# Performance work log

Hardware: AMD Instinct MI355X
Metric: run time of the kernel (lower is better)

## Reference

```python
import jax, jax.numpy as jnp
import numpy as np

B = 8            # graphs per batch (batch_size)
NPG = 4096       # nodes per graph
EPG = 65536      # edges per graph (avg degree 16)
IN = 384
K1, K2, K3 = 2458, 1475, 738   # ceil(.6*4096), ceil(.6*2458), ceil(.5*1475)
EPS = 1e-5


def setup_inputs() -> dict:
    key = jax.random.key(0)
    ks = jax.random.split(key, 16)
    x = jax.random.normal(ks[0], (B * NPG, IN), jnp.float32)
    off = (jnp.arange(B, dtype=jnp.int32) * NPG)[:, None]
    src = jax.random.randint(ks[1], (B, EPG), 0, NPG, dtype=jnp.int32) + off
    dst = jax.random.randint(ks[2], (B, EPG), 0, NPG, dtype=jnp.int32) + off
    edge_index = jnp.stack([src.reshape(-1), dst.reshape(-1)])

    def lin(k, i, o):
        return jax.random.normal(k, (i, o), jnp.float32) / np.sqrt(i)

    return dict(
        x=x, edge_index=edge_index,
        W1=lin(ks[3], IN, 512), b1=jnp.zeros(512, jnp.float32),
        W2=lin(ks[4], 512, 512), b2=jnp.zeros(512, jnp.float32),
        W3=lin(ks[5], 512, 256), b3=jnp.zeros(256, jnp.float32),
        W4=lin(ks[6], 256, 192), b4=jnp.zeros(192, jnp.float32),
        g1=jnp.ones(512, jnp.float32), be1=jnp.zeros(512, jnp.float32),
        g2=jnp.ones(512, jnp.float32), be2=jnp.zeros(512, jnp.float32),
        g3=jnp.ones(256, jnp.float32), be3=jnp.zeros(256, jnp.float32),
        p1_wrel=lin(ks[7], 512, 1), p1_brel=jnp.zeros(1, jnp.float32), p1_wroot=lin(ks[8], 512, 1),
        p2_wrel=lin(ks[9], 512, 1), p2_brel=jnp.zeros(1, jnp.float32), p2_wroot=lin(ks[10], 512, 1),
        p3_wrel=lin(ks[11], 256, 1), p3_brel=jnp.zeros(1, jnp.float32), p3_wroot=lin(ks[12], 256, 1),
    )


def _gcn_conv(x, W, b, src, dst, em, n):
    # PyG GCNConv(add_self_loops=False): h = D^-1/2 A D^-1/2 (x W) + b
    h = x @ W
    deg = jax.ops.segment_sum(em, dst, num_segments=n)           # in-degree of valid edges
    dis = jnp.where(deg > 0, jax.lax.rsqrt(jnp.maximum(deg, 1e-12)), 0.0)
    norm = (dis[src] * dis[dst] * em)[:, None]
    return jax.ops.segment_sum(h[src] * norm, dst, num_segments=n) + b


def _bn(x, g, b):
    # BatchNorm(track_running_stats=False): always batch stats, biased var
    mu = jnp.mean(x, axis=0)
    var = jnp.mean(jnp.square(x - mu), axis=0)
    return (x - mu) * jax.lax.rsqrt(var + EPS) * g + b


def _sag_score(x, wrel, brel, wroot, src, dst, em, n):
    # SAGPooling's GNN = GraphConv: lin_rel(sum_j x_j) + lin_root(x)
    agg = jax.ops.segment_sum(x[src] * em[:, None], dst, num_segments=n)
    return (agg @ wrel + brel + x @ wroot)[:, 0]


def _sag_pool(x, score, src, dst, em, npg, k):
    # per-graph top-k on raw scores; kept features scaled by tanh(score)
    topv, topi = jax.lax.top_k(score.reshape(B, npg), k)
    perm = (topi + (jnp.arange(B, dtype=jnp.int32) * npg)[:, None]).reshape(-1)
    xn = x[perm] * jnp.tanh(topv.reshape(-1))[:, None]
    inv = jnp.full(B * npg, -1, jnp.int32).at[perm].set(
        jnp.arange(B * k, dtype=jnp.int32))
    ns, nd = inv[src], inv[dst]
    keep = (ns >= 0) & (nd >= 0)
    em = em * keep.astype(x.dtype)
    return xn, jnp.where(keep, ns, 0), jnp.where(keep, nd, 0), em


def reference(x, edge_index,
              W1, b1, W2, b2, W3, b3, W4, b4,
              g1, be1, g2, be2, g3, be3,
              p1_wrel, p1_brel, p1_wroot,
              p2_wrel, p2_brel, p2_wroot,
              p3_wrel, p3_brel, p3_wroot,
              batch_size=8):
    src, dst = edge_index[0], edge_index[1]
    em = jnp.ones(src.shape[0], x.dtype)

    h = jax.nn.relu(_bn(_gcn_conv(x, W1, b1, src, dst, em, B * NPG), g1, be1))
    s = _sag_score(h, p1_wrel, p1_brel, p1_wroot, src, dst, em, B * NPG)
    h, src, dst, em = _sag_pool(h, s, src, dst, em, NPG, K1)

    h = jax.nn.relu(_bn(_gcn_conv(h, W2, b2, src, dst, em, B * K1), g2, be2))
    s = _sag_score(h, p2_wrel, p2_brel, p2_wroot, src, dst, em, B * K1)
    h, src, dst, em = _sag_pool(h, s, src, dst, em, K1, K2)

    h = jax.nn.relu(_bn(_gcn_conv(h, W3, b3, src, dst, em, B * K2), g3, be3))
    s = _sag_score(h, p3_wrel, p3_brel, p3_wroot, src, dst, em, B * K2)
    h, src, dst, em = _sag_pool(h, s, src, dst, em, K2, K3)

    h = _gcn_conv(h, W4, b4, src, dst, em, B * K3)      # [B*K3, 192]
    hg = h.reshape(B, K3, 192)
    return jnp.mean(hg, axis=1) + jnp.max(hg, axis=1)   # global mean + max pool
```

## Files before the change

kernel.cpp:

```cpp
#include <hip/hip_runtime.h>
#include <cmath>

#define E_TOTAL 524288
#define NB 8

using f32x4 = __attribute__((ext_vector_type(4))) float;
using s16x8 = __attribute__((ext_vector_type(8))) short;
using s16x4 = __attribute__((ext_vector_type(4))) short;

static inline int cdiv(int a, int b) { return (a + b - 1) / b; }

__device__ inline unsigned short bf16_rn(float x) {
  unsigned u = __float_as_uint(x);
  return (unsigned short)((u + 0x7FFFu + ((u >> 16) & 1u)) >> 16);
}
__device__ inline void split3(float x, short& h, short& m, short& l) {
  unsigned short hb = bf16_rn(x);
  h = (short)hb;
  float hf = __uint_as_float(((unsigned)hb) << 16);
  float r1 = x - hf;
  unsigned short mb = bf16_rn(r1);
  m = (short)mb;
  float mf = __uint_as_float(((unsigned)mb) << 16);
  l = (short)bf16_rn(r1 - mf);
}

__device__ inline void async_copy16(const short* g, short* l) {
  __builtin_amdgcn_global_load_lds(
      (const __attribute__((address_space(1))) void*)(unsigned long long)(g),
      (__attribute__((address_space(3))) void*)(unsigned)(unsigned long long)(l),
      16, 0, 0);
}

__global__ void fill_i32(int* p, int v, int n) {
  int i = blockIdx.x * 256 + threadIdx.x;
  if (i < n) p[i] = v;
}

__global__ void split_w_t(const float* __restrict__ W, short* __restrict__ TH,
                          short* __restrict__ TM, short* __restrict__ TL, int K, int N) {
  int i = blockIdx.x * 256 + threadIdx.x;
  if (i >= K * N) return;
  int k = i / N, n = i % N;
  short h, m, l;
  split3(W[i], h, m, l);
  TH[(size_t)n * K + k] = h;
  TM[(size_t)n * K + k] = m;
  TL[(size_t)n * K + k] = l;
}

#define GBM 128
#define GBN 256
#define GBK 32
#define BUFS 36864
#define BOFF 12288

__global__ __launch_bounds__(512) void gemm_mfma(
    const short* __restrict__ AH, const short* __restrict__ AM, const short* __restrict__ AL,
    const short* __restrict__ BH, const short* __restrict__ BM, const short* __restrict__ BL,
    const float* __restrict__ bias, float* __restrict__ C,
    int M, int K, int N, int nblocks) {
  __shared__ __align__(16) short lds[2][BUFS];
  int nwg = gridDim.x;
  int orig = blockIdx.x;
  int q = nwg >> 3, r = nwg & 7;
  int xc = orig & 7, j8 = orig >> 3;
  int wg = (xc < r ? xc * (q + 1) : r * (q + 1) + (xc - r) * q) + j8;
  int bm = (wg / nblocks) * GBM;
  int bn = (wg % nblocks) * GBN;
  int tid = threadIdx.x;
  int wave = tid >> 6, lane = tid & 63;
  int wr = wave >> 2, wc = wave & 3;
  int l15 = lane & 15, l4 = lane >> 4;
  int pa = wave * 64 + lane;
  int ra = pa >> 2, ca = (pa & 3) ^ ((ra >> 1) & 3);
  int gar = bm + ra; gar = gar < M ? gar : 0;
  size_t gaoff = (size_t)gar * K + ca * 8;
  int adest = wave * 512;
  int pb0 = wave * 128 + lane, pb1 = pb0 + 64;
  int rb0 = pb0 >> 2, cb0 = (pb0 & 3) ^ ((rb0 >> 1) & 3);
  int rb1 = pb1 >> 2, cb1 = (pb1 & 3) ^ ((rb1 >> 1) & 3);
  int gbr0 = bn + rb0; gbr0 = gbr0 < N ? gbr0 : 0;
  int gbr1 = bn + rb1; gbr1 = gbr1 < N ? gbr1 : 0;
  size_t gboff0 = (size_t)gbr0 * K + cb0 * 8;
  size_t gboff1 = (size_t)gbr1 * K + cb1 * 8;
  int bdest = BOFF + wave * 1024;

  auto stage = [&](int b, int k0) {
    short* base = lds[b];
    async_copy16(AH + gaoff + k0, base + adest);
    async_copy16(AM + gaoff + k0, base + 4096 + adest);
    async_copy16(AL + gaoff + k0, base + 8192 + adest);
    async_copy16(BH + gboff0 + k0, base + bdest);
    async_copy16(BH + gboff1 + k0, base + bdest + 512);
    async_copy16(BM + gboff0 + k0, base + 8192 + bdest);
    async_copy16(BM + gboff1 + k0, base + 8192 + bdest + 512);
    async_copy16(BL + gboff0 + k0, base + 16384 + bdest);
    async_copy16(BL + gboff1 + k0, base + 16384 + bdest + 512);
  };

  f32x4 acc[4][4] = {};
  int cur = 0;
  stage(0, 0);
  __syncthreads();
  for (int k0 = 0; k0 < K; k0 += GBK) {
    if (k0 + GBK < K) stage(cur ^ 1, k0 + GBK);
    const short* base = lds[cur];
    s16x8 fah[4], fam[4], fal[4], fbh[4], fbm[4], fbl[4];
#pragma unroll
    for (int mi = 0; mi < 4; ++mi) {
      int row = wr * 64 + mi * 16 + l15;
      int ad = row * 32 + ((l4 ^ ((row >> 1) & 3)) << 3);
      fah[mi] = *(const s16x8*)(base + ad);
      fam[mi] = *(const s16x8*)(base + 4096 + ad);
      fal[mi] = *(const s16x8*)(base + 8192 + ad);
    }
#pragma unroll
    for (int ni = 0; ni < 4; ++ni) {
      int row = wc * 64 + ni * 16 + l15;
      int bd = BOFF + row * 32 + ((l4 ^ ((row >> 1) & 3)) << 3);
      fbh[ni] = *(const s16x8*)(base + bd);
      fbm[ni] = *(const s16x8*)(base + 8192 + bd);
      fbl[ni] = *(const s16x8*)(base + 16384 + bd);
    }
#pragma unroll
    for (int mi = 0; mi < 4; ++mi)
#pragma unroll
      for (int ni = 0; ni < 4; ++ni) {
        acc[mi][ni] = __builtin_amdgcn_mfma_f32_16x16x32_bf16(fah[mi], fbh[ni], acc[mi][ni], 0, 0, 0);
        acc[mi][ni] = __builtin_amdgcn_mfma_f32_16x16x32_bf16(fah[mi], fbm[ni], acc[mi][ni], 0, 0, 0);
        acc[mi][ni] = __builtin_amdgcn_mfma_f32_16x16x32_bf16(fam[mi], fbh[ni], acc[mi][ni], 0, 0, 0);
        acc[mi][ni] = __builtin_amdgcn_mfma_f32_16x16x32_bf16(fah[mi], fbl[ni], acc[mi][ni], 0, 0, 0);
        acc[mi][ni] = __builtin_amdgcn_mfma_f32_16x16x32_bf16(fal[mi], fbh[ni], acc[mi][ni], 0, 0, 0);
        acc[mi][ni] = __builtin_amdgcn_mfma_f32_16x16x32_bf16(fam[mi], fbm[ni], acc[mi][ni], 0, 0, 0);
      }
    __syncthreads();
    cur ^= 1;
  }
#pragma unroll
  for (int ni = 0; ni < 4; ++ni) {
    int col = bn + wc * 64 + ni * 16 + l15;
    if (col >= N) continue;
    float bv = bias ? bias[col] : 0.f;
#pragma unroll
    for (int mi = 0; mi < 4; ++mi) {
      int row0 = bm + wr * 64 + mi * 16 + l4 * 4;
#pragma unroll
      for (int rr = 0; rr < 4; ++rr) {
        int row = row0 + rr;
        if (row < M) C[(size_t)row * N + col] = acc[mi][ni][rr] + bv;
      }
    }
  }
}

__global__ void count_kernel(const int* __restrict__ dst, int* __restrict__ cnt, int E) {
  int e = blockIdx.x * 256 + threadIdx.x;
  if (e >= E) return;
  atomicAdd(&cnt[dst[e]], 1);
}

__global__ __launch_bounds__(1024) void scan_kernel(const int* __restrict__ cnt,
                                                    int* __restrict__ offs,
                                                    float* __restrict__ dis, int n) {
  __shared__ int tsum[1024];
  int tid = threadIdx.x;
  int chunk = (n + 1023) / 1024;
  int base = tid * chunk;
  int lsum = 0;
  for (int i = 0; i < chunk; ++i) {
    int idx = base + i;
    if (idx < n) lsum += cnt[idx];
  }
  tsum[tid] = lsum;
  __syncthreads();
  for (int off = 1; off < 1024; off <<= 1) {
    int add = (tid >= off) ? tsum[tid - off] : 0;
    __syncthreads();
    tsum[tid] += add;
    __syncthreads();
  }
  int run = (tid == 0) ? 0 : tsum[tid - 1];
  for (int i = 0; i < chunk; ++i) {
    int idx = base + i;
    if (idx < n) {
      offs[idx] = run;
      int c = cnt[idx];
      run += c;
      dis[idx] = (c > 0) ? (float)(1.0 / sqrt((double)c)) : 0.f;
    }
  }
  if (tid == 1023) offs[n] = run;
}

__global__ void scatter_kernel(const int* __restrict__ src, const int* __restrict__ dst,
                               const int* __restrict__ offs, int* __restrict__ tmpc,
                               int* __restrict__ esrc, int E) {
  int e = blockIdx.x * 256 + threadIdx.x;
  if (e >= E) return;
  int d = dst[e];
  if (d < 0) return;
  int pos = offs[d] + atomicAdd(&tmpc[d], 1);
  esrc[pos] = src[e];
}

__global__ void sort_buckets(const int* __restrict__ offs, int* __restrict__ esrc, int n) {
  int node = blockIdx.x * 256 + threadIdx.x;
  if (node >= n) return;
  int s0 = offs[node], s1 = offs[node + 1];
  for (int i = s0 + 1; i < s1; ++i) {
    int v = esrc[i];
    int j = i - 1;
    while (j >= s0 && esrc[j] > v) { esrc[j + 1] = esrc[j]; --j; }
    esrc[j + 1] = v;
  }
}

__global__ __launch_bounds__(256) void agg_kernel(
    const float* __restrict__ h, const int* __restrict__ offs,
    const int* __restrict__ esrc, const float* __restrict__ dis,
    const float* __restrict__ bias, float* __restrict__ outf,
    short* __restrict__ outh, short* __restrict__ outm, short* __restrict__ outl,
    int F, int n) {
  int node = blockIdx.x * 4 + (threadIdx.x >> 6);
  if (node >= n) return;
  int lane = threadIdx.x & 63;
  int nf4 = F >> 2;
  int i0 = lane, i1 = lane + 64;
  bool a0 = i0 < nf4, a1 = i1 < nf4;
  f32x4 acc0 = {}, acc1 = {};
  int e0 = offs[node], e1 = offs[node + 1];
  int e = e0;
  for (; e + 4 <= e1; e += 4) {
    int s0 = esrc[e], s1 = esrc[e + 1], s2 = esrc[e + 2], s3 = esrc[e + 3];
    float w0 = dis[s0], w1 = dis[s1], w2 = dis[s2], w3 = dis[s3];
    const f32x4* p0 = (const f32x4*)(h + (size_t)s0 * F);
    const f32x4* p1 = (const f32x4*)(h + (size_t)s1 * F);
    const f32x4* p2 = (const f32x4*)(h + (size_t)s2 * F);
    const f32x4* p3 = (const f32x4*)(h + (size_t)s3 * F);
    if (a0) {
      f32x4 v0 = p0[i0], v1 = p1[i0], v2 = p2[i0], v3 = p3[i0];
      acc0 += v0 * w0;
      acc0 += v1 * w1;
      acc0 += v2 * w2;
      acc0 += v3 * w3;
    }
    if (a1) {
      f32x4 v0 = p0[i1], v1 = p1[i1], v2 = p2[i1], v3 = p3[i1];
      acc1 += v0 * w0;
      acc1 += v1 * w1;
      acc1 += v2 * w2;
      acc1 += v3 * w3;
    }
  }
  for (; e < e1; ++e) {
    int s = esrc[e];
    float w = dis[s];
    const f32x4* hp = (const f32x4*)(h + (size_t)s * F);
    if (a0) acc0 += hp[i0] * w;
    if (a1) acc1 += hp[i1] * w;
  }
  float wd = dis[node];
  acc0 *= wd;
  acc1 *= wd;
  if (outf) {
    const f32x4* b4 = (const f32x4*)bias;
    f32x4* op = (f32x4*)(outf + (size_t)node * F);
    if (a0) op[i0] = acc0 + b4[i0];
    if (a1) op[i1] = acc1 + b4[i1];
  } else {
    short hh[4], mm[4], ll[4];
    if (a0) {
#pragma unroll
      for (int c = 0; c < 4; ++c) split3(acc0[c], hh[c], mm[c], ll[c]);
      *(s16x4*)&outh[(size_t)node * F + i0 * 4] = *(s16x4*)hh;
      *(s16x4*)&outm[(size_t)node * F + i0 * 4] = *(s16x4*)mm;
      *(s16x4*)&outl[(size_t)node * F + i0 * 4] = *(s16x4*)ll;
    }
    if (a1) {
#pragma unroll
      for (int c = 0; c < 4; ++c) split3(acc1[c], hh[c], mm[c], ll[c]);
      *(s16x4*)&outh[(size_t)node * F + i1 * 4] = *(s16x4*)hh;
      *(s16x4*)&outm[(size_t)node * F + i1 * 4] = *(s16x4*)mm;
      *(s16x4*)&outl[(size_t)node * F + i1 * 4] = *(s16x4*)ll;
    }
  }
}

#define BNY 512
__global__ void bn_stats_part(const float* __restrict__ x, double* __restrict__ psum,
                              double* __restrict__ psq, int n, int F) {
  int col = blockIdx.x * 256 + threadIdx.x;
  if (col >= F) return;
  double s = 0., q = 0.;
  for (int r = blockIdx.y; r < n; r += gridDim.y) {
    double v = (double)x[(size_t)r * F + col];
    s += v;
    q += v * v;
  }
  psum[blockIdx.y * F + col] = s;
  psq[blockIdx.y * F + col] = q;
}

__global__ __launch_bounds__(64) void bn_reduce(
    const double* __restrict__ psum, const double* __restrict__ psq,
    const float* __restrict__ g, const float* __restrict__ be,
    float* __restrict__ scf, float* __restrict__ shf,
    double* __restrict__ scd, double* __restrict__ shd, int n, int F) {
  int c = blockIdx.x;
  int lane = threadIdx.x;
  double s = 0., q = 0.;
  for (int p = lane; p < BNY; p += 64) {
    s += psum[p * F + c];
    q += psq[p * F + c];
  }
#pragma unroll
  for (int o = 1; o < 64; o <<= 1) {
    s += __shfl_xor(s, o, 64);
    q += __shfl_xor(q, o, 64);
  }
  if (lane == 0) {
    double inv_n = 1.0 / (double)n;
    double mu = s * inv_n;
    double var = q * inv_n - mu * mu;
    if (var < 0.) var = 0.;
    double istd = 1.0 / sqrt(var + 1e-5);
    double sc = istd * (double)g[c];
    double sh = (double)be[c] - mu * sc;
    scd[c] = sc;
    shd[c] = sh;
    scf[c] = (float)sc;
    shf[c] = (float)sh;
  }
}

__global__ __launch_bounds__(256) void bn_apply_score(
    float* __restrict__ hx, const float* __restrict__ scf, const float* __restrict__ shf,
    const double* __restrict__ scd, const double* __restrict__ shd,
    const float* __restrict__ wrel, const float* __restrict__ wroot,
    double* __restrict__ t, double* __restrict__ r, int F, int n) {
  int row = blockIdx.x * 4 + (threadIdx.x >> 6);
  if (row >= n) return;
  int lane = threadIdx.x & 63;
  int nf4 = F >> 2;
  f32x4* hp = (f32x4*)(hx + (size_t)row * F);
  const f32x4* sc = (const f32x4*)scf;
  const f32x4* sh = (const f32x4*)shf;
  double dr = 0., dq = 0.;
  for (int j = lane; j < nf4; j += 64) {
    f32x4 hv = hp[j];
    f32x4 v = hv * sc[j] + sh[j];
#pragma unroll
    for (int c = 0; c < 4; ++c) v[c] = fmaxf(v[c], 0.f);
    hp[j] = v;
#pragma unroll
    for (int c = 0; c < 4; ++c) {
      double vd = (double)hv[c] * scd[j * 4 + c] + shd[j * 4 + c];
      vd = vd > 0. ? vd : 0.;
      dr += vd * (double)wrel[j * 4 + c];
      dq += vd * (double)wroot[j * 4 + c];
    }
  }
#pragma unroll
  for (int o = 1; o < 64; o <<= 1) {
    dr += __shfl_xor(dr, o, 64);
    dq += __shfl_xor(dq, o, 64);
  }
  if (lane == 0) { t[row] = dr; r[row] = dq; }
}

__global__ void score_kernel(const int* __restrict__ offs, const int* __restrict__ esrc,
                             const double* __restrict__ t, const double* __restrict__ r,
                             const float* __restrict__ brel, double* __restrict__ s, int n) {
  int i = blockIdx.x * 256 + threadIdx.x;
  if (i >= n) return;
  double acc = 0.;
  int e0 = offs[i], e1 = offs[i + 1];
  for (int e = e0; e < e1; ++e) acc += t[esrc[e]];
  s[i] = acc + r[i] + (double)brel[0];
}

__global__ __launch_bounds__(1024) void topk_kernel(
    const double* __restrict__ s, int n_pg, int k, int npad,
    int* __restrict__ perm, float* __restrict__ tanhv, int* __restrict__ inv) {
  extern __shared__ char smem[];
  unsigned long long* sk = (unsigned long long*)smem;
  unsigned* si = (unsigned*)(smem + (size_t)npad * 8);
  int g = blockIdx.x;
  for (int i = threadIdx.x; i < n_pg; i += blockDim.x)
    inv[(size_t)g * n_pg + i] = -1;
  for (int i = threadIdx.x; i < npad; i += blockDim.x) {
    if (i < n_pg) {
      double v = s[(size_t)g * n_pg + i];
      unsigned long long u = (unsigned long long)__double_as_longlong(v);
      u = (u >> 63) ? ~u : (u | 0x8000000000000000ULL);
      sk[i] = ~u;
      si[i] = (unsigned)i;
    } else {
      sk[i] = 0xFFFFFFFFFFFFFFFFULL;
      si[i] = 0xFFFFFFFFu;
    }
  }
  __syncthreads();
  for (int size = 2; size <= npad; size <<= 1) {
    for (int stride = size >> 1; stride > 0; stride >>= 1) {
      for (int t = threadIdx.x; t < (npad >> 1); t += blockDim.x) {
        int i = ((t / stride) * stride * 2) + (t % stride);
        int j = i + stride;
        bool up = ((i & size) == 0);
        unsigned long long ka = sk[i], kb = sk[j];
        unsigned ia = si[i], ib = si[j];
        bool sw = up ? ((ka > kb) || (ka == kb && ia > ib))
                     : ((ka < kb) || (ka == kb && ia < ib));
        if (sw) { sk[i] = kb; sk[j] = ka; si[i] = ib; si[j] = ia; }
      }
      __syncthreads();
    }
  }
  for (int j = threadIdx.x; j < k; j += blockDim.x) {
    int li = (int)si[j];
    int old_g = g * n_pg + li;
    int new_g = g * k + j;
    perm[new_g] = old_g;
    tanhv[new_g] = (float)tanh(s[old_g]);
    inv[old_g] = new_g;
  }
}

__global__ __launch_bounds__(256) void gather_split(
    const float* __restrict__ h, const int* __restrict__ perm,
    const float* __restrict__ tanhv, short* __restrict__ gh, short* __restrict__ gm,
    short* __restrict__ gl, int F, int nk) {
  int i = blockIdx.x * 4 + (threadIdx.x >> 6);
  if (i >= nk) return;
  int lane = threadIdx.x & 63;
  int nf4 = F >> 2;
  int p = perm[i];
  float tv = tanhv[i];
  const f32x4* hp = (const f32x4*)(h + (size_t)p * F);
  for (int j = lane; j < nf4; j += 64) {
    f32x4 v = hp[j] * tv;
    short hh[4], mm[4], ll[4];
#pragma unroll
    for (int c = 0; c < 4; ++c) split3(v[c], hh[c], mm[c], ll[c]);
    *(s16x4*)&gh[(size_t)i * F + j * 4] = *(s16x4*)hh;
    *(s16x4*)&gm[(size_t)i * F + j * 4] = *(s16x4*)mm;
    *(s16x4*)&gl[(size_t)i * F + j * 4] = *(s16x4*)ll;
  }
}

__global__ void remap_kernel(const int* __restrict__ src_in, const int* __restrict__ dst_in,
                             const int* __restrict__ inv, int* __restrict__ src_out,
                             int* __restrict__ dst_out, int* __restrict__ cnt, int E) {
  int e = blockIdx.x * 256 + threadIdx.x;
  if (e >= E) return;
  int d = dst_in[e];
  int ns = -1, nd = -1;
  if (d >= 0) { ns = inv[src_in[e]]; nd = inv[d]; }
  if (ns >= 0 && nd >= 0) {
    src_out[e] = ns;
    dst_out[e] = nd;
    atomicAdd(&cnt[nd], 1);
  } else {
    src_out[e] = 0;
    dst_out[e] = -1;
  }
}

#define PCH 16
__global__ void pool_partial(const float* __restrict__ h, float* __restrict__ part,
                             int k3, int F) {
  int g = blockIdx.x, c = blockIdx.y;
  int tid = threadIdx.x;
  int chunk = (k3 + PCH - 1) / PCH;
  int r0 = c * chunk, r1 = min(r0 + chunk, k3);
  const float* base = h + (size_t)g * k3 * F;
  float sm = 0.f, mx = -INFINITY;
  for (int r = r0; r < r1; ++r) {
    float v = base[(size_t)r * F + tid];
    sm += v;
    mx = fmaxf(mx, v);
  }
  float* pp = part + (size_t)(g * PCH + c) * 2 * F;
  pp[tid] = sm;
  pp[F + tid] = mx;
}
__global__ void pool_final(const float* __restrict__ part, float* __restrict__ out,
                           int k3, int F) {
  int g = blockIdx.x;
  int tid = threadIdx.x;
  float sm = 0.f, mx = -INFINITY;
  for (int c = 0; c < PCH; ++c) {
    const float* pp = part + (size_t)(g * PCH + c) * 2 * F;
    sm += pp[tid];
    mx = fmaxf(mx, pp[F + tid]);
  }
  out[g * F + tid] = sm / (float)k3 + mx;
}

extern "C" void kernel_launch(void* const* d_in, const int* in_sizes, int n_in,
                              void* d_out, int out_size, void* d_ws, size_t ws_size,
                              hipStream_t stream) {
  const float* x0 = (const float*)d_in[0];
  const int* eidx = (const int*)d_in[1];
  const float* W1 = (const float*)d_in[2];  const float* b1 = (const float*)d_in[3];
  const float* W2 = (const float*)d_in[4];  const float* b2 = (const float*)d_in[5];
  const float* W3 = (const float*)d_in[6];  const float* b3 = (const float*)d_in[7];
  const float* W4 = (const float*)d_in[8];  const float* b4 = (const float*)d_in[9];
  const float* g1 = (const float*)d_in[10]; const float* be1 = (const float*)d_in[11];
  const float* g2 = (const float*)d_in[12]; const float* be2 = (const float*)d_in[13];
  const float* g3 = (const float*)d_in[14]; const float* be3 = (const float*)d_in[15];
  const float* p1r = (const float*)d_in[16]; const float* p1b = (const float*)d_in[17];
  const float* p1o = (const float*)d_in[18];
  const float* p2r = (const float*)d_in[19]; const float* p2b = (const float*)d_in[20];
  const float* p2o = (const float*)d_in[21];
  const float* p3r = (const float*)d_in[22]; const float* p3b = (const float*)d_in[23];
  const float* p3o = (const float*)d_in[24];

  char* w = (char*)d_ws;
  size_t off = 0;
  auto alloc = [&](size_t bytes) -> void* {
    void* p = w + off;
    off = (off + bytes + 255) & ~(size_t)255;
    return p;
  };
  float* BUF0 = (float*)alloc(32768ull * 512 * 4);
  float* BUF1 = (float*)alloc(19664ull * 512 * 4);
  short* XH = (short*)alloc(32768ull * 384 * 2);
  short* XM = (short*)alloc(32768ull * 384 * 2);
  short* XL = (short*)alloc(32768ull * 384 * 2);
  short* WTH = (short*)alloc(638976ull * 2);
  short* WTM = (short*)alloc(638976ull * 2);
  short* WTL = (short*)alloc(638976ull * 2);
  int* czone = (int*)alloc(65537ull * 4);
  int* cnt = czone;
  int* tmpc = czone + 32769;
  int* offs = (int*)alloc(32769 * 4);
  float* dis = (float*)alloc(32768 * 4);
  double* tvec = (double*)alloc(32768 * 8);
  double* rvec = (double*)alloc(32768 * 8);
  double* svec = (double*)alloc(32768 * 8);
  int* inv = (int*)alloc(32768 * 4);
  int* perm = (int*)alloc(32768 * 4);
  float* tanhv = (float*)alloc(32768 * 4);
  int* e0s = (int*)alloc(E_TOTAL * 4);
  int* e0d = (int*)alloc(E_TOTAL * 4);
  int* e1s = (int*)alloc(E_TOTAL * 4);
  int* e1d = (int*)alloc(E_TOTAL * 4);
  int* esrc = (int*)alloc(E_TOTAL * 4);
  double* bnsum = (double*)alloc((size_t)BNY * 512 * 8);
  double* bnsq = (double*)alloc((size_t)BNY * 512 * 8);
  float* bnscf = (float*)alloc(512 * 4);
  float* bnshf = (float*)alloc(512 * 4);
  double* bnscd = (double*)alloc(512 * 8);
  double* bnshd = (double*)alloc(512 * 8);
  float* part = (float*)alloc((size_t)NB * PCH * 2 * 192 * 4);

  const int EB = cdiv(E_TOTAL, 256);

  auto build_csr = [&](const int* src, const int* dst, int n) {
    scan_kernel<<<1, 1024, 0, stream>>>(cnt, offs, dis, n);
    scatter_kernel<<<EB, 256, 0, stream>>>(src, dst, offs, tmpc, esrc, E_TOTAL);
    sort_buckets<<<cdiv(n, 256), 256, 0, stream>>>(offs, esrc, n);
  };

  auto pool = [&](float* hbuf, int n, int n_pg, int k, int npad, int F,
                  const float* g, const float* be, const float* wr, const float* wb,
                  const float* wo, const int* src, const int* dst, int* nsrc, int* ndst) {
    bn_stats_part<<<dim3(cdiv(F, 256), BNY), 256, 0, stream>>>(hbuf, bnsum, bnsq, n, F);
    bn_reduce<<<F, 64, 0, stream>>>(bnsum, bnsq, g, be, bnscf, bnshf, bnscd, bnshd, n, F);
    bn_apply_score<<<cdiv(n, 4), 256, 0, stream>>>(hbuf, bnscf, bnshf, bnscd, bnshd, wr, wo, tvec, rvec, F, n);
    score_kernel<<<cdiv(n, 256), 256, 0, stream>>>(offs, esrc, tvec, rvec, wb, svec, n);
    topk_kernel<<<NB, 1024, (size_t)npad * 12, stream>>>(svec, n_pg, k, npad, perm, tanhv, inv);
    gather_split<<<cdiv(NB * k, 4), 256, 0, stream>>>(hbuf, perm, tanhv, XH, XM, XL, F, NB * k);
    fill_i32<<<cdiv(65537, 256), 256, 0, stream>>>(czone, 0, 65537);
    remap_kernel<<<EB, 256, 0, stream>>>(src, dst, inv, nsrc, ndst, cnt, E_TOTAL);
  };

  split_w_t<<<cdiv(384 * 512, 256), 256, 0, stream>>>(W1, WTH, WTM, WTL, 384, 512);
  split_w_t<<<cdiv(512 * 512, 256), 256, 0, stream>>>(W2, WTH + 196608, WTM + 196608, WTL + 196608, 512, 512);
  split_w_t<<<cdiv(512 * 256, 256), 256, 0, stream>>>(W3, WTH + 458752, WTM + 458752, WTL + 458752, 512, 256);
  split_w_t<<<cdiv(256 * 192, 256), 256, 0, stream>>>(W4, WTH + 589824, WTM + 589824, WTL + 589824, 256, 192);

  fill_i32<<<cdiv(65537, 256), 256, 0, stream>>>(czone, 0, 65537);
  count_kernel<<<EB, 256, 0, stream>>>(eidx + E_TOTAL, cnt, E_TOTAL);
  build_csr(eidx, eidx + E_TOTAL, 32768);
  agg_kernel<<<cdiv(32768, 4), 256, 0, stream>>>(x0, offs, esrc, dis, nullptr, nullptr, XH, XM, XL, 384, 32768);
  gemm_mfma<<<cdiv(32768, 128) * 2, 512, 0, stream>>>(XH, XM, XL, WTH, WTM, WTL, b1, BUF0, 32768, 384, 512, 2);
  pool(BUF0, 32768, 4096, 2458, 4096, 512, g1, be1, p1r, p1b, p1o, eidx, eidx + E_TOTAL, e0s, e0d);

  build_csr(e0s, e0d, 19664);
  gemm_mfma<<<cdiv(19664, 128) * 2, 512, 0, stream>>>(XH, XM, XL, WTH + 196608, WTM + 196608, WTL + 196608, nullptr, BUF0, 19664, 512, 512, 2);
  agg_kernel<<<cdiv(19664, 4), 256, 0, stream>>>(BUF0, offs, esrc, dis, b2, BUF1, nullptr, nullptr, nullptr, 512, 19664);
  pool(BUF1, 19664, 2458, 1475, 4096, 512, g2, be2, p2r, p2b, p2o, e0s, e0d, e1s, e1d);

  build_csr(e1s, e1d, 11800);
  gemm_mfma<<<cdiv(11800, 128), 512, 0, stream>>>(XH, XM, XL, WTH + 458752, WTM + 458752, WTL + 458752, nullptr, BUF0, 11800, 512, 256, 1);
  agg_kernel<<<cdiv(11800, 4), 256, 0, stream>>>(BUF0, offs, esrc, dis, b3, BUF1, nullptr, nullptr, nullptr, 256, 11800);
  pool(BUF1, 11800, 1475, 738, 2048, 256, g3, be3, p3r, p3b, p3o, e1s, e1d, e0s, e0d);

  build_csr(e0s, e0d, 5904);
  gemm_mfma<<<cdiv(5904, 128), 512, 0, stream>>>(XH, XM, XL, WTH + 589824, WTM + 589824, WTL + 589824, nullptr, BUF0, 5904, 256, 192, 1);
  agg_kernel<<<cdiv(5904, 4), 256, 0, stream>>>(BUF0, offs, esrc, dis, b4, BUF1, nullptr, nullptr, nullptr, 192, 5904);
  pool_partial<<<dim3(NB, PCH), 192, 0, stream>>>(BUF1, part, 738, 192);
  pool_final<<<NB, 192, 0, stream>>>(part, (float*)d_out, 738, 192);
}
```

Baseline: 1.139 ms.

## Replace bitonic-sort top-k with radix select and ordered compaction

The full bitonic sort of per-graph scores in shared memory is replaced by an 8-pass, 8-bit radix select that finds the k-th largest key. The selected nodes are then compacted in index order with a block-wide prefix scan. This removes the many barrier-separated sort stages and the large dynamic shared-memory allocation. In exchange, the kept nodes come out in index order instead of score order, which should not change the permutation-invariant final output. The low 12 mantissa bits of each score are also overwritten by the node index as a tie-breaker, which slightly alters how near-ties are resolved.

```diff
diff --git a/kernel.cpp b/kernel.cpp
--- a/kernel.cpp
+++ b/kernel.cpp
@@ -380,50 +380,91 @@
   s[i] = acc + r[i] + (double)brel[0];
 }
 
-__global__ __launch_bounds__(1024) void topk_kernel(
-    const double* __restrict__ s, int n_pg, int k, int npad,
+__global__ __launch_bounds__(1024) void topk_select(
+    const double* __restrict__ s, int n_pg, int k,
     int* __restrict__ perm, float* __restrict__ tanhv, int* __restrict__ inv) {
-  extern __shared__ char smem[];
-  unsigned long long* sk = (unsigned long long*)smem;
-  unsigned* si = (unsigned*)(smem + (size_t)npad * 8);
+  __shared__ unsigned hist[256];
+  __shared__ unsigned long long sPfx;
+  __shared__ int sRem;
+  __shared__ unsigned wsum[16];
   int g = blockIdx.x;
-  for (int i = threadIdx.x; i < n_pg; i += blockDim.x)
-    inv[(size_t)g * n_pg + i] = -1;
-  for (int i = threadIdx.x; i < npad; i += blockDim.x) {
-    if (i < n_pg) {
-      double v = s[(size_t)g * n_pg + i];
-      unsigned long long u = (unsigned long long)__double_as_longlong(v);
-      u = (u >> 63) ? ~u : (u | 0x8000000000000000ULL);
-      sk[i] = ~u;
-      si[i] = (unsigned)i;
+  int tid = threadIdx.x;
+  const double* sg = s + (size_t)g * n_pg;
+  auto keyof = [&](int i) -> unsigned long long {
+    unsigned long long u = (unsigned long long)__double_as_longlong(sg[i]);
+    u = (u >> 63) ? ~u : (u | 0x8000000000000000ULL);
+    return ((u >> 12) << 12) | (unsigned long long)(4095 - i);
+  };
+  unsigned long long prefix = 0;
+  int rem = k;
+  for (int shift = 56; shift >= 0; shift -= 8) {
+    if (tid < 256) hist[tid] = 0;
+    __syncthreads();
+    unsigned long long himask = (shift == 56) ? 0ULL : (~0ULL << (shift + 8));
+    for (int i = tid; i < n_pg; i += 1024) {
+      unsigned long long kk = keyof(i);
+      if ((kk & himask) == prefix) {
+        unsigned b = (unsigned)((kk >> shift) & 255);
+        atomicAdd(&hist[b], 1u);
+      }
+    }
+    __syncthreads();
+    if (tid == 0) {
+      int rr = rem;
+      unsigned long long pfx = prefix;
+      for (int b = 255; b >= 0; --b) {
+        int c = (int)hist[b];
+        if (c < rr) { rr -= c; }
+        else { pfx |= ((unsigned long long)b) << shift; break; }
+      }
+      sPfx = pfx;
+      sRem = rr;
+    }
+    __syncthreads();
+    prefix = sPfx;
+    rem = sRem;
+    __syncthreads();
+  }
+  unsigned long long Kstar = prefix;
+  int c = (n_pg + 1023) / 1024;
+  int base = tid * c;
+  int loc[4];
+  int cnt = 0;
+#pragma unroll 4
+  for (int j = 0; j < c; ++j) {
+    int i = base + j;
+    int sel = (i < n_pg && keyof(i) >= Kstar) ? 1 : 0;
+    loc[j] = cnt;
+    cnt += sel;
+  }
+  int lane = tid & 63, wid = tid >> 6;
+  int v = cnt;
+  for (int o = 1; o < 64; o <<= 1) {
+    int u2 = __shfl_up(v, o, 64);
+    if (lane >= o) v += u2;
+  }
+  int wexcl = v - cnt;
+  if (lane == 63) wsum[wid] = (unsigned)v;
+  __syncthreads();
+  if (tid == 0) {
+    unsigned run = 0;
+    for (int wi = 0; wi < 16; ++wi) { unsigned t2 = wsum[wi]; wsum[wi] = run; run += t2; }
+  }
+  __syncthreads();
+  int offset = (int)wsum[wid] + wexcl;
+  for (int j = 0; j < c; ++j) {
+    int i = base + j;
+    if (i >= n_pg) break;
+    bool sel = keyof(i) >= Kstar;
+    int old_g = g * n_pg + i;
+    if (sel) {
+      int new_g = g * k + offset + loc[j];
+      perm[new_g] = old_g;
+      tanhv[new_g] = (float)tanh(sg[i]);
+      inv[old_g] = new_g;
     } else {
-      sk[i] = 0xFFFFFFFFFFFFFFFFULL;
-      si[i] = 0xFFFFFFFFu;
-    }
-  }
-  __syncthreads();
-  for (int size = 2; size <= npad; size <<= 1) {
-    for (int stride = size >> 1; stride > 0; stride >>= 1) {
-      for (int t = threadIdx.x; t < (npad >> 1); t += blockDim.x) {
-        int i = ((t / stride) * stride * 2) + (t % stride);
-        int j = i + stride;
-        bool up = ((i & size) == 0);
-        unsigned long long ka = sk[i], kb = sk[j];
-        unsigned ia = si[i], ib = si[j];
-        bool sw = up ? ((ka > kb) || (ka == kb && ia > ib))
-                     : ((ka < kb) || (ka == kb && ia < ib));
-        if (sw) { sk[i] = kb; sk[j] = ka; si[i] = ib; si[j] = ia; }
-      }
-      __syncthreads();
-    }
-  }
-  for (int j = threadIdx.x; j < k; j += blockDim.x) {
-    int li = (int)si[j];
-    int old_g = g * n_pg + li;
-    int new_g = g * k + j;
-    perm[new_g] = old_g;
-    tanhv[new_g] = (float)tanh(s[old_g]);
-    inv[old_g] = new_g;
+      inv[old_g] = -1;
+    }
   }
 }
 
@@ -564,14 +605,14 @@
     sort_buckets<<<cdiv(n, 256), 256, 0, stream>>>(offs, esrc, n);
   };
 
-  auto pool = [&](float* hbuf, int n, int n_pg, int k, int npad, int F,
+  auto pool = [&](float* hbuf, int n, int n_pg, int k, int F,
                   const float* g, const float* be, const float* wr, const float* wb,
                   const float* wo, const int* src, const int* dst, int* nsrc, int* ndst) {
     bn_stats_part<<<dim3(cdiv(F, 256), BNY), 256, 0, stream>>>(hbuf, bnsum, bnsq, n, F);
     bn_reduce<<<F, 64, 0, stream>>>(bnsum, bnsq, g, be, bnscf, bnshf, bnscd, bnshd, n, F);
     bn_apply_score<<<cdiv(n, 4), 256, 0, stream>>>(hbuf, bnscf, bnshf, bnscd, bnshd, wr, wo, tvec, rvec, F, n);
     score_kernel<<<cdiv(n, 256), 256, 0, stream>>>(offs, esrc, tvec, rvec, wb, svec, n);
-    topk_kernel<<<NB, 1024, (size_t)npad * 12, stream>>>(svec, n_pg, k, npad, perm, tanhv, inv);
+    topk_select<<<NB, 1024, 0, stream>>>(svec, n_pg, k, perm, tanhv, inv);
     gather_split<<<cdiv(NB * k, 4), 256, 0, stream>>>(hbuf, perm, tanhv, XH, XM, XL, F, NB * k);
     fill_i32<<<cdiv(65537, 256), 256, 0, stream>>>(czone, 0, 65537);
     remap_kernel<<<EB, 256, 0, stream>>>(src, dst, inv, nsrc, ndst, cnt, E_TOTAL);
@@ -587,17 +628,17 @@
   build_csr(eidx, eidx + E_TOTAL, 32768);
   agg_kernel<<<cdiv(32768, 4), 256, 0, stream>>>(x0, offs, esrc, dis, nullptr, nullptr, XH, XM, XL, 384, 32768);
   gemm_mfma<<<cdiv(32768, 128) * 2, 512, 0, stream>>>(XH, XM, XL, WTH, WTM, WTL, b1, BUF0, 32768, 384, 512, 2);
-  pool(BUF0, 32768, 4096, 2458, 4096, 512, g1, be1, p1r, p1b, p1o, eidx, eidx + E_TOTAL, e0s, e0d);
+  pool(BUF0, 32768, 4096, 2458, 512, g1, be1, p1r, p1b, p1o, eidx, eidx + E_TOTAL, e0s, e0d);
 
   build_csr(e0s, e0d, 19664);
   gemm_mfma<<<cdiv(19664, 128) * 2, 512, 0, stream>>>(XH, XM, XL, WTH + 196608, WTM + 196608, WTL + 196608, nullptr, BUF0, 19664, 512, 512, 2);
   agg_kernel<<<cdiv(19664, 4), 256, 0, stream>>>(BUF0, offs, esrc, dis, b2, BUF1, nullptr, nullptr, nullptr, 512, 19664);
-  pool(BUF1, 19664, 2458, 1475, 4096, 512, g2, be2, p2r, p2b, p2o, e0s, e0d, e1s, e1d);
+  pool(BUF1, 19664, 2458, 1475, 512, g2, be2, p2r, p2b, p2o, e0s, e0d, e1s, e1d);
 
   build_csr(e1s, e1d, 11800);
   gemm_mfma<<<cdiv(11800, 128), 512, 0, stream>>>(XH, XM, XL, WTH + 458752, WTM + 458752, WTL + 458752, nullptr, BUF0, 11800, 512, 256, 1);
   agg_kernel<<<cdiv(11800, 4), 256, 0, stream>>>(BUF0, offs, esrc, dis, b3, BUF1, nullptr, nullptr, nullptr, 256, 11800);
-  pool(BUF1, 11800, 1475, 738, 2048, 256, g3, be3, p3r, p3b, p3o, e1s, e1d, e0s, e0d);
+  pool(BUF1, 11800, 1475, 738, 256, g3, be3, p3r, p3b, p3o, e1s, e1d, e0s, e0d);
 
   build_csr(e0s, e0d, 5904);
   gemm_mfma<<<cdiv(5904, 128), 512, 0, stream>>>(XH, XM, XL, WTH + 589824, WTM + 589824, WTL + 589824, nullptr, BUF0, 5904, 256, 192, 1);
```

Result: faster. 1.102 ms (-3.3%).
